# Optimization experiments

Hardware: AMD Instinct MI355X
Metric: run time of the kernel (lower is better)

Reference implementation:

```python
import jax, jax.numpy as jnp
import numpy as np
from jax import lax


def setup_inputs() -> dict:
    key = jax.random.key(0)
    k1, k2 = jax.random.split(key)
    B, H, W, Cin, Cout, kh, kw = 16, 128, 128, 128, 128, 3, 3
    X = jax.random.normal(k1, (B, H, W, Cin), dtype=jnp.float32)
    kernel = jax.random.normal(k2, (B, kh, kw, Cin, Cout), dtype=jnp.float32) * 0.05
    return {"X": X, "kernel": kernel}


def _conv_one(x, k):
    # x: [H, W, Cin]; k: [kh, kw, Cin, Cout] -> [H', W', Cout]
    out = lax.conv_general_dilated(
        x[None],  # [1, H, W, Cin]
        k,
        window_strides=(1, 1),
        padding='VALID',
        dimension_numbers=('NHWC', 'HWIO', 'NHWC'),
    )
    return out[0]


def reference(X, kernel):
    # Per-sample dynamic-filter conv: each batch element convolved with its own
    # [kh, kw, Cin, Cout] filter. Equivalent to the TF depthwise-reshape trick
    # followed by reduce_sum over the input-channel axis.
    return jax.vmap(_conv_one)(X, kernel)  # [B, H', W', Cout]
```

## Files before the change

### kernel.cpp

```cpp
#include <hip/hip_runtime.h>
#include <cstdint>

#define OWD 126
#define MTOT 15876

typedef short bf16x8 __attribute__((ext_vector_type(8)));
typedef float f32x4  __attribute__((ext_vector_type(4)));

#define BT_ELEMS  (16u * 128u * 1152u)
#define XBF_ELEMS (16u * 128u * 128u * 128u)
#define WS_NEEDED ((size_t)(BT_ELEMS + XBF_ELEMS) * 2)

__device__ __forceinline__ uint16_t f2bf(float f) {
    union { float f; uint32_t u; } v;
    v.f = f;
    uint32_t u = v.u;
    return (uint16_t)((u + 0x7FFFu + ((u >> 16) & 1u)) >> 16);
}

__device__ __forceinline__ uint32_t pk2(float a, float b) {
    return (uint32_t)f2bf(a) | ((uint32_t)f2bf(b) << 16);
}

__device__ __forceinline__ void gl_lds16(const uint16_t* g, uint16_t* l) {
    __builtin_amdgcn_global_load_lds(
        (const __attribute__((address_space(1))) uint32_t*)g,
        (__attribute__((address_space(3))) uint32_t*)l, 16, 0, 0);
}

__global__ __launch_bounds__(256) void kprep(const float* __restrict__ Kin,
                                             uint16_t* __restrict__ Bt) {
    const int rs = blockIdx.x;
    const int b  = blockIdx.y;
    const int t  = threadIdx.x;
    const int n  = t & 127;
    const int og = t >> 7;

    const float* src = Kin + (((size_t)b * 9 + rs) << 14);
    uint16_t*    dst = Bt + ((size_t)b * 128 + n) * 1152 + rs * 128;

#pragma unroll
    for (int o = 0; o < 8; ++o) {
        const int oct = og * 8 + o;
        const float* s0 = src + (oct * 8) * 128 + n;
        uint4 p;
        p.x = pk2(s0[0 * 128], s0[1 * 128]);
        p.y = pk2(s0[2 * 128], s0[3 * 128]);
        p.z = pk2(s0[4 * 128], s0[5 * 128]);
        p.w = pk2(s0[6 * 128], s0[7 * 128]);
        *(uint4*)(dst + oct * 8) = p;
    }
}

__global__ __launch_bounds__(256) void xprep(const float* __restrict__ X,
                                             uint16_t* __restrict__ Xbf) {
    const size_t i = ((size_t)blockIdx.x * 256 + threadIdx.x) * 8;
    const float4 a = *(const float4*)(X + i);
    const float4 b = *(const float4*)(X + i + 4);
    uint4 p;
    p.x = pk2(a.x, a.y);
    p.y = pk2(a.z, a.w);
    p.z = pk2(b.x, b.y);
    p.w = pk2(b.z, b.w);
    *(uint4*)(Xbf + i) = p;
}

__global__ __launch_bounds__(256) void conv_mfma_a(const uint16_t* __restrict__ Xbf,
                                                   const uint16_t* __restrict__ Bt,
                                                   float* __restrict__ Out) {
    __shared__ __align__(16) uint16_t lA[2][128 * 64];
    __shared__ __align__(16) uint16_t lB[2][128 * 64];

    const int mtile = blockIdx.x;
    const int b     = blockIdx.y;
    const int tid   = threadIdx.x;
    const int lane  = tid & 63;
    const int wave  = tid >> 6;
    const int wm    = (wave & 1) << 6;
    const int wn    = (wave >> 1) << 6;
    const int l15   = lane & 15;
    const int quad  = lane >> 4;

    const int kc = (lane & 7) ^ (lane >> 3);
    const uint16_t* Asrc[4];
    const uint16_t* Bsrc[4];
#pragma unroll
    for (int i = 0; i < 4; ++i) {
        const int row = wave * 32 + i * 8 + (lane >> 3);
        int m = mtile * 128 + row;
        if (m >= MTOT) m = MTOT - 1;
        const int oh = m / OWD, ow = m - oh * OWD;
        Asrc[i] = Xbf + (((size_t)b * 128 + oh) * 128 + ow) * 128 + kc * 8;
        Bsrc[i] = Bt + ((size_t)b * 128 + row) * 1152 + kc * 8;
    }
    const int dbase = (wave * 256 + lane) * 8;

    f32x4 acc[4][4];
#pragma unroll
    for (int i = 0; i < 4; ++i)
#pragma unroll
        for (int j = 0; j < 4; ++j)
            acc[i][j] = (f32x4){0.f, 0.f, 0.f, 0.f};

#define STAGE(t_, bu_)                                                      \
    {                                                                       \
        const int rs_ = (t_) >> 1;                                         \
        const int c0_ = ((t_) & 1) << 6;                                   \
        const int r_  = (rs_ * 11) >> 5;                \
        const int s_  = rs_ - r_ * 3;                                      \
        const int ao_ = (r_ * 128 + s_) * 128 + c0_;                       \
        const int bo_ = rs_ * 128 + c0_;                                   \
        uint16_t* Ad_ = &lA[bu_][dbase];                                   \
        uint16_t* Bd_ = &lB[bu_][dbase];                                   \
        _Pragma("unroll")                                                  \
        for (int i_ = 0; i_ < 4; ++i_) {                                   \
            gl_lds16(Asrc[i_] + ao_, Ad_ + i_ * 512);                      \
            gl_lds16(Bsrc[i_] + bo_, Bd_ + i_ * 512);                      \
        }                                                                  \
    }

#define COMPUTE(bu_)                                                        \
    {                                                                       \
        _Pragma("unroll")                                                  \
        for (int ksub_ = 0; ksub_ < 2; ++ksub_) {                          \
            bf16x8 af[4], bfr[4];                                          \
            _Pragma("unroll")                                              \
            for (int i_ = 0; i_ < 4; ++i_) {                               \
                const int row_ = wm + i_ * 16 + l15;                       \
                const int pc_  = (ksub_ * 4 + quad) ^ (row_ & 7);          \
                af[i_] = *(const bf16x8*)&lA[bu_][row_ * 64 + pc_ * 8];    \
            }                                                              \
            _Pragma("unroll")                                              \
            for (int j_ = 0; j_ < 4; ++j_) {                               \
                const int row_ = wn + j_ * 16 + l15;                       \
                const int pc_  = (ksub_ * 4 + quad) ^ (row_ & 7);          \
                bfr[j_] = *(const bf16x8*)&lB[bu_][row_ * 64 + pc_ * 8];   \
            }                                                              \
            _Pragma("unroll")                                              \
            for (int i_ = 0; i_ < 4; ++i_)                                 \
                _Pragma("unroll")                                          \
                for (int j_ = 0; j_ < 4; ++j_)                             \
                    acc[i_][j_] = __builtin_amdgcn_mfma_f32_16x16x32_bf16( \
                        af[i_], bfr[j_], acc[i_][j_], 0, 0, 0);            \
        }                                                                  \
    }

    STAGE(0, 0);
    __syncthreads();

#pragma unroll 1
    for (int t = 0; t < 16; t += 2) {
        STAGE(t + 1, 1);
        COMPUTE(0);
        __syncthreads();
        STAGE(t + 2, 0);
        COMPUTE(1);
        __syncthreads();
    }
    STAGE(17, 1);
    COMPUTE(0);
    __syncthreads();
    COMPUTE(1);

#undef STAGE
#undef COMPUTE

#pragma unroll
    for (int i = 0; i < 4; ++i) {
#pragma unroll
        for (int rr = 0; rr < 4; ++rr) {
            const int mrow = mtile * 128 + wm + i * 16 + quad * 4 + rr;
            if (mrow < MTOT) {
                const int oh2 = mrow / OWD;
                const int ow2 = mrow - oh2 * OWD;
                float* op = Out + (((size_t)b * OWD + oh2) * OWD + ow2) * 128 + wn + l15;
#pragma unroll
                for (int j = 0; j < 4; ++j)
                    op[j * 16] = acc[i][j][rr];
            }
        }
    }
}

__global__ __launch_bounds__(256) void conv_mfma(const float* __restrict__ X,
                                                 const uint16_t* __restrict__ Bt,
                                                 float* __restrict__ Out) {
    __shared__ __align__(16) uint16_t lA[128 * 64];
    __shared__ __align__(16) uint16_t lB[128 * 64];

    const int mtile = blockIdx.x;
    const int b     = blockIdx.y;
    const int tid   = threadIdx.x;
    const int lane  = tid & 63;
    const int wave  = tid >> 6;
    const int wm    = (wave & 1) << 6;
    const int wn    = (wave >> 1) << 6;
    const int l15   = lane & 15;
    const int quad  = lane >> 4;

    const int srow  = tid >> 1;
    const int shalf = tid & 1;

    int m = mtile * 128 + srow;
    if (m >= MTOT) m = MTOT - 1;
    const int oh = m / OWD;
    const int ow = m - oh * OWD;
    const float*    Xb = X + (((size_t)b * 128 + oh) * 128 + ow) * 128;
    const uint16_t* Bb = Bt + ((size_t)b * 128 + srow) * 1152 + shalf * 32;

    f32x4 acc[4][4];
#pragma unroll
    for (int i = 0; i < 4; ++i)
#pragma unroll
        for (int j = 0; j < 4; ++j)
            acc[i][j] = (f32x4){0.f, 0.f, 0.f, 0.f};

    for (int chunk = 0; chunk < 18; ++chunk) {
        const int rs = chunk >> 1;
        const int c0 = (chunk & 1) << 6;
        const int r  = rs / 3;
        const int s  = rs - r * 3;

        __syncthreads();
        {
            const float4* src = (const float4*)(Xb + (r * 128 + s) * 128 + c0 + shalf * 32);
            float4 v[8];
#pragma unroll
            for (int i = 0; i < 8; ++i) v[i] = src[i];
#pragma unroll
            for (int i = 0; i < 4; ++i) {
                uint4 p;
                p.x = pk2(v[2 * i].x, v[2 * i].y);
                p.y = pk2(v[2 * i].z, v[2 * i].w);
                p.z = pk2(v[2 * i + 1].x, v[2 * i + 1].y);
                p.w = pk2(v[2 * i + 1].z, v[2 * i + 1].w);
                const int ci = (shalf * 4 + i) ^ (srow & 7);
                *(uint4*)&lA[srow * 64 + ci * 8] = p;
            }
        }
        {
            const uint4* bsrc = (const uint4*)(Bb + rs * 128 + c0);
#pragma unroll
            for (int i = 0; i < 4; ++i) {
                const uint4 p = bsrc[i];
                const int ci = (shalf * 4 + i) ^ (srow & 7);
                *(uint4*)&lB[srow * 64 + ci * 8] = p;
            }
        }
        __syncthreads();

#pragma unroll
        for (int ksub = 0; ksub < 2; ++ksub) {
            bf16x8 af[4], bfr[4];
#pragma unroll
            for (int i = 0; i < 4; ++i) {
                const int row = wm + i * 16 + l15;
                const int ci  = (ksub * 4 + quad) ^ (row & 7);
                af[i] = *(const bf16x8*)&lA[row * 64 + ci * 8];
            }
#pragma unroll
            for (int j = 0; j < 4; ++j) {
                const int row = wn + j * 16 + l15;
                const int ci  = (ksub * 4 + quad) ^ (row & 7);
                bfr[j] = *(const bf16x8*)&lB[row * 64 + ci * 8];
            }
#pragma unroll
            for (int i = 0; i < 4; ++i)
#pragma unroll
                for (int j = 0; j < 4; ++j)
                    acc[i][j] = __builtin_amdgcn_mfma_f32_16x16x32_bf16(
                        af[i], bfr[j], acc[i][j], 0, 0, 0);
        }
    }

#pragma unroll
    for (int i = 0; i < 4; ++i) {
#pragma unroll
        for (int rr = 0; rr < 4; ++rr) {
            const int mrow = mtile * 128 + wm + i * 16 + quad * 4 + rr;
            if (mrow < MTOT) {
                const int oh2 = mrow / OWD;
                const int ow2 = mrow - oh2 * OWD;
                float* op = Out + (((size_t)b * OWD + oh2) * OWD + ow2) * 128 + wn + l15;
#pragma unroll
                for (int j = 0; j < 4; ++j)
                    op[j * 16] = acc[i][j][rr];
            }
        }
    }
}

extern "C" void kernel_launch(void* const* d_in, const int* in_sizes, int n_in,
                              void* d_out, int out_size, void* d_ws, size_t ws_size,
                              hipStream_t stream) {
    const float* X   = (const float*)d_in[0];
    const float* Kin = (const float*)d_in[1];
    float*       Out = (float*)d_out;
    uint16_t*    Bt  = (uint16_t*)d_ws;
    uint16_t*    Xbf = Bt + BT_ELEMS;

    kprep<<<dim3(9, 16), 256, 0, stream>>>(Kin, Bt);
    if (ws_size >= WS_NEEDED) {
        xprep<<<XBF_ELEMS / (256 * 8), 256, 0, stream>>>(X, Xbf);
        conv_mfma_a<<<dim3(125, 16), 256, 0, stream>>>(Xbf, Bt, Out);
    } else {
        conv_mfma<<<dim3(125, 16), 256, 0, stream>>>(X, Bt, Out);
    }
}
```

Baseline: 324.6 us.

## Enlarge M tile to 256 and load B fragments directly into registers

Result: slower. 347.6 us (+7.1%).

```diff
diff --git a/kernel.cpp b/kernel.cpp
--- a/kernel.cpp
+++ b/kernel.cpp
@@ -65,11 +65,142 @@
     *(uint4*)(Xbf + i) = p;
 }
 
-__global__ __launch_bounds__(256) void conv_mfma_a(const uint16_t* __restrict__ Xbf,
-                                                   const uint16_t* __restrict__ Bt,
-                                                   float* __restrict__ Out) {
-    __shared__ __align__(16) uint16_t lA[2][128 * 64];
-    __shared__ __align__(16) uint16_t lB[2][128 * 64];
+__global__ __launch_bounds__(256, 2) void conv_mfma_b(const uint16_t* __restrict__ Xbf,
+                                                      const uint16_t* __restrict__ Bt,
+                                                      float* __restrict__ Out) {
+    __shared__ __align__(16) uint16_t lA[2][256 * 64];
+
+    const int mtile = blockIdx.x;
+    const int b     = blockIdx.y;
+    const int tid   = threadIdx.x;
+    const int lane  = tid & 63;
+    const int wave  = tid >> 6;
+    const int wm    = (wave & 1) << 7;
+    const int wn    = (wave >> 1) << 6;
+    const int l15   = lane & 15;
+    const int quad  = lane >> 4;
+
+    const int kc = (lane & 7) ^ (lane >> 3);
+    const uint16_t* Asrc[8];
+#pragma unroll
+    for (int i = 0; i < 8; ++i) {
+        const int row = wave * 64 + i * 8 + (lane >> 3);
+        int m = mtile * 256 + row;
+        if (m >= MTOT) m = MTOT - 1;
+        const int oh = m / OWD, ow = m - oh * OWD;
+        Asrc[i] = Xbf + (((size_t)b * 128 + oh) * 128 + ow) * 128 + kc * 8;
+    }
+    uint16_t* Ad0 = &lA[0][(wave * 512 + lane) * 8];
+    uint16_t* Ad1 = &lA[1][(wave * 512 + lane) * 8];
+
+    const uint16_t* Bp[4];
+#pragma unroll
+    for (int j = 0; j < 4; ++j)
+        Bp[j] = Bt + ((size_t)b * 128 + wn + j * 16 + l15) * 1152 + quad * 8;
+
+    f32x4 acc[8][4];
+#pragma unroll
+    for (int i = 0; i < 8; ++i)
+#pragma unroll
+        for (int j = 0; j < 4; ++j)
+            acc[i][j] = (f32x4){0.f, 0.f, 0.f, 0.f};
+
+    bf16x8 bA[8], bB[8];
+
+#define STAGE(t_, Ad_)                                                      \
+    {                                                                       \
+        const int rs_ = (t_) >> 1;                                         \
+        const int c0_ = ((t_) & 1) << 6;                                   \
+        const int r_  = (rs_ * 11) >> 5;                \
+        const int s_  = rs_ - r_ * 3;                                      \
+        const int ao_ = (r_ * 128 + s_) * 128 + c0_;                       \
+        _Pragma("unroll")                                                  \
+        for (int i_ = 0; i_ < 8; ++i_)                                     \
+            gl_lds16(Asrc[i_] + ao_, Ad_ + i_ * 512);                      \
+    }
+
+#define LOADB(t_, br_)                                                      \
+    {                                                                       \
+        const int off_ = ((t_) >> 1) * 128 + (((t_) & 1) << 6);            \
+        _Pragma("unroll")                                                  \
+        for (int j_ = 0; j_ < 4; ++j_) {                                   \
+            br_[j_ * 2 + 0] = *(const bf16x8*)(Bp[j_] + off_);             \
+            br_[j_ * 2 + 1] = *(const bf16x8*)(Bp[j_] + off_ + 32);        \
+        }                                                                  \
+    }
+
+#define COMPUTE(bu_, br_)                                                   \
+    {                                                                       \
+        _Pragma("unroll")                                                  \
+        for (int ksub_ = 0; ksub_ < 2; ++ksub_) {                          \
+            _Pragma("unroll")                                              \
+            for (int ih_ = 0; ih_ < 2; ++ih_) {                            \
+                bf16x8 af[4];                                              \
+                _Pragma("unroll")                                          \
+                for (int i_ = 0; i_ < 4; ++i_) {                           \
+                    const int row_ = wm + (ih_ * 4 + i_) * 16 + l15;       \
+                    const int pc_  = (ksub_ * 4 + quad) ^ (row_ & 7);      \
+                    af[i_] = *(const bf16x8*)&lA[bu_][row_ * 64 + pc_ * 8];\
+                }                                                          \
+                _Pragma("unroll")                                          \
+                for (int i_ = 0; i_ < 4; ++i_)                             \
+                    _Pragma("unroll")                                      \
+                    for (int j_ = 0; j_ < 4; ++j_)                         \
+                        acc[ih_ * 4 + i_][j_] =                            \
+                            __builtin_amdgcn_mfma_f32_16x16x32_bf16(       \
+                                af[i_], br_[j_ * 2 + ksub_],               \
+                                acc[ih_ * 4 + i_][j_], 0, 0, 0);           \
+            }                                                              \
+        }                                                                  \
+    }
+
+    LOADB(0, bA);
+    STAGE(0, Ad0);
+    __syncthreads();
+
+#pragma unroll 1
+    for (int t = 0; t < 16; t += 2) {
+        LOADB(t + 1, bB);
+        STAGE(t + 1, Ad1);
+        COMPUTE(0, bA);
+        __syncthreads();
+        LOADB(t + 2, bA);
+        STAGE(t + 2, Ad0);
+        COMPUTE(1, bB);
+        __syncthreads();
+    }
+    LOADB(17, bB);
+    STAGE(17, Ad1);
+    COMPUTE(0, bA);
+    __syncthreads();
+    COMPUTE(1, bB);
+
+#undef STAGE
+#undef LOADB
+#undef COMPUTE
+
+#pragma unroll
+    for (int i = 0; i < 8; ++i) {
+#pragma unroll
+        for (int rr = 0; rr < 4; ++rr) {
+            const int mrow = mtile * 256 + wm + i * 16 + quad * 4 + rr;
+            if (mrow < MTOT) {
+                const int oh2 = mrow / OWD;
+                const int ow2 = mrow - oh2 * OWD;
+                float* op = Out + (((size_t)b * OWD + oh2) * OWD + ow2) * 128 + wn + l15;
+#pragma unroll
+                for (int j = 0; j < 4; ++j)
+                    op[j * 16] = acc[i][j][rr];
+            }
+        }
+    }
+}
+
+__global__ __launch_bounds__(256) void conv_mfma(const float* __restrict__ X,
+                                                 const uint16_t* __restrict__ Bt,
+                                                 float* __restrict__ Out) {
+    __shared__ __align__(16) uint16_t lA[128 * 64];
+    __shared__ __align__(16) uint16_t lB[128 * 64];
 
     const int mtile = blockIdx.x;
     const int b     = blockIdx.y;
@@ -81,123 +212,6 @@
     const int l15   = lane & 15;
     const int quad  = lane >> 4;
 
-    const int kc = (lane & 7) ^ (lane >> 3);
-    const uint16_t* Asrc[4];
-    const uint16_t* Bsrc[4];
-#pragma unroll
-    for (int i = 0; i < 4; ++i) {
-        const int row = wave * 32 + i * 8 + (lane >> 3);
-        int m = mtile * 128 + row;
-        if (m >= MTOT) m = MTOT - 1;
-        const int oh = m / OWD, ow = m - oh * OWD;
-        Asrc[i] = Xbf + (((size_t)b * 128 + oh) * 128 + ow) * 128 + kc * 8;
-        Bsrc[i] = Bt + ((size_t)b * 128 + row) * 1152 + kc * 8;
-    }
-    const int dbase = (wave * 256 + lane) * 8;
-
-    f32x4 acc[4][4];
-#pragma unroll
-    for (int i = 0; i < 4; ++i)
-#pragma unroll
-        for (int j = 0; j < 4; ++j)
-            acc[i][j] = (f32x4){0.f, 0.f, 0.f, 0.f};
-
-#define STAGE(t_, bu_)                                                      \
-    {                                                                       \
-        const int rs_ = (t_) >> 1;                                         \
-        const int c0_ = ((t_) & 1) << 6;                                   \
-        const int r_  = (rs_ * 11) >> 5;                \
-        const int s_  = rs_ - r_ * 3;                                      \
-        const int ao_ = (r_ * 128 + s_) * 128 + c0_;                       \
-        const int bo_ = rs_ * 128 + c0_;                                   \
-        uint16_t* Ad_ = &lA[bu_][dbase];                                   \
-        uint16_t* Bd_ = &lB[bu_][dbase];                                   \
-        _Pragma("unroll")                                                  \
-        for (int i_ = 0; i_ < 4; ++i_) {                                   \
-            gl_lds16(Asrc[i_] + ao_, Ad_ + i_ * 512);                      \
-            gl_lds16(Bsrc[i_] + bo_, Bd_ + i_ * 512);                      \
-        }                                                                  \
-    }
-
-#define COMPUTE(bu_)                                                        \
-    {                                                                       \
-        _Pragma("unroll")                                                  \
-        for (int ksub_ = 0; ksub_ < 2; ++ksub_) {                          \
-            bf16x8 af[4], bfr[4];                                          \
-            _Pragma("unroll")                                              \
-            for (int i_ = 0; i_ < 4; ++i_) {                               \
-                const int row_ = wm + i_ * 16 + l15;                       \
-                const int pc_  = (ksub_ * 4 + quad) ^ (row_ & 7);          \
-                af[i_] = *(const bf16x8*)&lA[bu_][row_ * 64 + pc_ * 8];    \
-            }                                                              \
-            _Pragma("unroll")                                              \
-            for (int j_ = 0; j_ < 4; ++j_) {                               \
-                const int row_ = wn + j_ * 16 + l15;                       \
-                const int pc_  = (ksub_ * 4 + quad) ^ (row_ & 7);          \
-                bfr[j_] = *(const bf16x8*)&lB[bu_][row_ * 64 + pc_ * 8];   \
-            }                                                              \
-            _Pragma("unroll")                                              \
-            for (int i_ = 0; i_ < 4; ++i_)                                 \
-                _Pragma("unroll")                                          \
-                for (int j_ = 0; j_ < 4; ++j_)                             \
-                    acc[i_][j_] = __builtin_amdgcn_mfma_f32_16x16x32_bf16( \
-                        af[i_], bfr[j_], acc[i_][j_], 0, 0, 0);            \
-        }                                                                  \
-    }
-
-    STAGE(0, 0);
-    __syncthreads();
-
-#pragma unroll 1
-    for (int t = 0; t < 16; t += 2) {
-        STAGE(t + 1, 1);
-        COMPUTE(0);
-        __syncthreads();
-        STAGE(t + 2, 0);
-        COMPUTE(1);
-        __syncthreads();
-    }
-    STAGE(17, 1);
-    COMPUTE(0);
-    __syncthreads();
-    COMPUTE(1);
-
-#undef STAGE
-#undef COMPUTE
-
-#pragma unroll
-    for (int i = 0; i < 4; ++i) {
-#pragma unroll
-        for (int rr = 0; rr < 4; ++rr) {
-            const int mrow = mtile * 128 + wm + i * 16 + quad * 4 + rr;
-            if (mrow < MTOT) {
-                const int oh2 = mrow / OWD;
-                const int ow2 = mrow - oh2 * OWD;
-                float* op = Out + (((size_t)b * OWD + oh2) * OWD + ow2) * 128 + wn + l15;
-#pragma unroll
-                for (int j = 0; j < 4; ++j)
-                    op[j * 16] = acc[i][j][rr];
-            }
-        }
-    }
-}
-
-__global__ __launch_bounds__(256) void conv_mfma(const float* __restrict__ X,
-                                                 const uint16_t* __restrict__ Bt,
-                                                 float* __restrict__ Out) {
-    __shared__ __align__(16) uint16_t lA[128 * 64];
-    __shared__ __align__(16) uint16_t lB[128 * 64];
-
-    const int mtile = blockIdx.x;
-    const int b     = blockIdx.y;
-    const int tid   = threadIdx.x;
-    const int lane  = tid & 63;
-    const int wave  = tid >> 6;
-    const int wm    = (wave & 1) << 6;
-    const int wn    = (wave >> 1) << 6;
-    const int l15   = lane & 15;
-    const int quad  = lane >> 4;
-
     const int srow  = tid >> 1;
     const int shalf = tid & 1;
 
@@ -302,7 +316,7 @@
     kprep<<<dim3(9, 16), 256, 0, stream>>>(Kin, Bt);
     if (ws_size >= WS_NEEDED) {
         xprep<<<XBF_ELEMS / (256 * 8), 256, 0, stream>>>(X, Xbf);
-        conv_mfma_a<<<dim3(125, 16), 256, 0, stream>>>(Xbf, Bt, Out);
+        conv_mfma_b<<<dim3(63, 16), 256, 0, stream>>>(Xbf, Bt, Out);
     } else {
         conv_mfma<<<dim3(125, 16), 256, 0, stream>>>(X, Bt, Out);
     }
```

## Use triple-buffered K=32 LDS pipeline with vmcnt waits and XCD-aware block remap

Applied to the files above, without the earlier changes.

Result: no change. 325.8 us (+0.4%).

```diff
diff --git a/kernel.cpp b/kernel.cpp
--- a/kernel.cpp
+++ b/kernel.cpp
@@ -65,11 +65,142 @@
     *(uint4*)(Xbf + i) = p;
 }
 
-__global__ __launch_bounds__(256) void conv_mfma_a(const uint16_t* __restrict__ Xbf,
+__global__ __launch_bounds__(256) void conv_mfma_c(const uint16_t* __restrict__ Xbf,
                                                    const uint16_t* __restrict__ Bt,
                                                    float* __restrict__ Out) {
-    __shared__ __align__(16) uint16_t lA[2][128 * 64];
-    __shared__ __align__(16) uint16_t lB[2][128 * 64];
+    __shared__ __align__(16) uint16_t lds[3][256 * 32];
+
+    const int id    = blockIdx.x + 125 * blockIdx.y;
+    const int nid   = (id & 7) * 250 + (id >> 3);
+    const int mtile = nid % 125;
+    const int b     = nid / 125;
+
+    const int tid  = threadIdx.x;
+    const int lane = tid & 63;
+    const int wave = tid >> 6;
+    const int wm   = (wave & 1) << 6;
+    const int wn   = (wave >> 1) << 6;
+    const int l15  = lane & 15;
+    const int quad = lane >> 4;
+
+    const int l2 = lane >> 2;
+    const int kc = (lane & 3) ^ (l2 & 3);
+    const uint16_t* Asrc[2];
+    const uint16_t* Bsrc[2];
+#pragma unroll
+    for (int i = 0; i < 2; ++i) {
+        const int row = wave * 32 + i * 16 + l2;
+        int m = mtile * 128 + row;
+        if (m >= MTOT) m = MTOT - 1;
+        const int oh = m / OWD, ow = m - oh * OWD;
+        Asrc[i] = Xbf + (((size_t)b * 128 + oh) * 128 + ow) * 128 + kc * 8;
+        Bsrc[i] = Bt + ((size_t)b * 128 + row) * 1152 + kc * 8;
+    }
+    const int dbase = wave * 1024 + lane * 8;
+
+    f32x4 acc[4][4];
+#pragma unroll
+    for (int i = 0; i < 4; ++i)
+#pragma unroll
+        for (int j = 0; j < 4; ++j)
+            acc[i][j] = (f32x4){0.f, 0.f, 0.f, 0.f};
+
+#define STAGE(t_, bu_)                                                      \
+    {                                                                       \
+        const int rs_ = (t_) >> 2;                                         \
+        const int c0_ = ((t_) & 3) << 5;                                   \
+        const int r_  = (rs_ * 11) >> 5;                \
+        const int s_  = rs_ - r_ * 3;                                      \
+        const int ao_ = (r_ * 128 + s_) * 128 + c0_;                       \
+        const int bo_ = rs_ * 128 + c0_;                                   \
+        uint16_t* Ad_ = &lds[bu_][dbase];                                  \
+        uint16_t* Bd_ = &lds[bu_][4096 + dbase];                           \
+        _Pragma("unroll")                                                  \
+        for (int i_ = 0; i_ < 2; ++i_) {                                   \
+            gl_lds16(Asrc[i_] + ao_, Ad_ + i_ * 512);                      \
+            gl_lds16(Bsrc[i_] + bo_, Bd_ + i_ * 512);                      \
+        }                                                                  \
+    }
+
+#define COMPUTE(bu_)                                                        \
+    {                                                                       \
+        bf16x8 af[4], bfr[4];                                              \
+        _Pragma("unroll")                                                  \
+        for (int i_ = 0; i_ < 4; ++i_) {                                   \
+            const int row_ = wm + i_ * 16 + l15;                           \
+            const int sl_  = quad ^ (row_ & 3);                            \
+            af[i_] = *(const bf16x8*)&lds[bu_][row_ * 32 + sl_ * 8];       \
+        }                                                                  \
+        _Pragma("unroll")                                                  \
+        for (int j_ = 0; j_ < 4; ++j_) {                                   \
+            const int row_ = wn + j_ * 16 + l15;                           \
+            const int sl_  = quad ^ (row_ & 3);                            \
+            bfr[j_] = *(const bf16x8*)&lds[bu_][4096 + row_ * 32 + sl_ * 8];\
+        }                                                                  \
+        _Pragma("unroll")                                                  \
+        for (int i_ = 0; i_ < 4; ++i_)                                     \
+            _Pragma("unroll")                                              \
+            for (int j_ = 0; j_ < 4; ++j_)                                 \
+                acc[i_][j_] = __builtin_amdgcn_mfma_f32_16x16x32_bf16(     \
+                    af[i_], bfr[j_], acc[i_][j_], 0, 0, 0);                \
+    }
+
+#define WAITBAR4                                                            \
+    asm volatile("s_waitcnt vmcnt(4)" ::: "memory");                       \
+    __builtin_amdgcn_s_barrier();                                          \
+    __builtin_amdgcn_sched_barrier(0);
+
+#define ITER(t_, bc_, bs_)                                                  \
+    {                                                                       \
+        WAITBAR4;                                                          \
+        STAGE((t_) + 2, bs_);                                              \
+        COMPUTE(bc_);                                                      \
+    }
+
+    STAGE(0, 0);
+    STAGE(1, 1);
+
+#pragma unroll 1
+    for (int t = 0; t < 33; t += 3) {
+        ITER(t, 0, 2);
+        ITER(t + 1, 1, 0);
+        ITER(t + 2, 2, 1);
+    }
+    ITER(33, 0, 2);
+    WAITBAR4;
+    COMPUTE(1);
+    asm volatile("s_waitcnt vmcnt(0)" ::: "memory");
+    __builtin_amdgcn_s_barrier();
+    __builtin_amdgcn_sched_barrier(0);
+    COMPUTE(2);
+
+#undef STAGE
+#undef COMPUTE
+#undef WAITBAR4
+#undef ITER
+
+#pragma unroll
+    for (int i = 0; i < 4; ++i) {
+#pragma unroll
+        for (int rr = 0; rr < 4; ++rr) {
+            const int mrow = mtile * 128 + wm + i * 16 + quad * 4 + rr;
+            if (mrow < MTOT) {
+                const int oh2 = mrow / OWD;
+                const int ow2 = mrow - oh2 * OWD;
+                float* op = Out + (((size_t)b * OWD + oh2) * OWD + ow2) * 128 + wn + l15;
+#pragma unroll
+                for (int j = 0; j < 4; ++j)
+                    op[j * 16] = acc[i][j][rr];
+            }
+        }
+    }
+}
+
+__global__ __launch_bounds__(256) void conv_mfma(const float* __restrict__ X,
+                                                 const uint16_t* __restrict__ Bt,
+                                                 float* __restrict__ Out) {
+    __shared__ __align__(16) uint16_t lA[128 * 64];
+    __shared__ __align__(16) uint16_t lB[128 * 64];
 
     const int mtile = blockIdx.x;
     const int b     = blockIdx.y;
@@ -81,123 +212,6 @@
     const int l15   = lane & 15;
     const int quad  = lane >> 4;
 
-    const int kc = (lane & 7) ^ (lane >> 3);
-    const uint16_t* Asrc[4];
-    const uint16_t* Bsrc[4];
-#pragma unroll
-    for (int i = 0; i < 4; ++i) {
-        const int row = wave * 32 + i * 8 + (lane >> 3);
-        int m = mtile * 128 + row;
-        if (m >= MTOT) m = MTOT - 1;
-        const int oh = m / OWD, ow = m - oh * OWD;
-        Asrc[i] = Xbf + (((size_t)b * 128 + oh) * 128 + ow) * 128 + kc * 8;
-        Bsrc[i] = Bt + ((size_t)b * 128 + row) * 1152 + kc * 8;
-    }
-    const int dbase = (wave * 256 + lane) * 8;
-
-    f32x4 acc[4][4];
-#pragma unroll
-    for (int i = 0; i < 4; ++i)
-#pragma unroll
-        for (int j = 0; j < 4; ++j)
-            acc[i][j] = (f32x4){0.f, 0.f, 0.f, 0.f};
-
-#define STAGE(t_, bu_)                                                      \
-    {                                                                       \
-        const int rs_ = (t_) >> 1;                                         \
-        const int c0_ = ((t_) & 1) << 6;                                   \
-        const int r_  = (rs_ * 11) >> 5;                \
-        const int s_  = rs_ - r_ * 3;                                      \
-        const int ao_ = (r_ * 128 + s_) * 128 + c0_;                       \
-        const int bo_ = rs_ * 128 + c0_;                                   \
-        uint16_t* Ad_ = &lA[bu_][dbase];                                   \
-        uint16_t* Bd_ = &lB[bu_][dbase];                                   \
-        _Pragma("unroll")                                                  \
-        for (int i_ = 0; i_ < 4; ++i_) {                                   \
-            gl_lds16(Asrc[i_] + ao_, Ad_ + i_ * 512);                      \
-            gl_lds16(Bsrc[i_] + bo_, Bd_ + i_ * 512);                      \
-        }                                                                  \
-    }
-
-#define COMPUTE(bu_)                                                        \
-    {                                                                       \
-        _Pragma("unroll")                                                  \
-        for (int ksub_ = 0; ksub_ < 2; ++ksub_) {                          \
-            bf16x8 af[4], bfr[4];                                          \
-            _Pragma("unroll")                                              \
-            for (int i_ = 0; i_ < 4; ++i_) {                               \
-                const int row_ = wm + i_ * 16 + l15;                       \
-                const int pc_  = (ksub_ * 4 + quad) ^ (row_ & 7);          \
-                af[i_] = *(const bf16x8*)&lA[bu_][row_ * 64 + pc_ * 8];    \
-            }                                                              \
-            _Pragma("unroll")                                              \
-            for (int j_ = 0; j_ < 4; ++j_) {                               \
-                const int row_ = wn + j_ * 16 + l15;                       \
-                const int pc_  = (ksub_ * 4 + quad) ^ (row_ & 7);          \
-                bfr[j_] = *(const bf16x8*)&lB[bu_][row_ * 64 + pc_ * 8];   \
-            }                                                              \
-            _Pragma("unroll")                                              \
-            for (int i_ = 0; i_ < 4; ++i_)                                 \
-                _Pragma("unroll")                                          \
-                for (int j_ = 0; j_ < 4; ++j_)                             \
-                    acc[i_][j_] = __builtin_amdgcn_mfma_f32_16x16x32_bf16( \
-                        af[i_], bfr[j_], acc[i_][j_], 0, 0, 0);            \
-        }                                                                  \
-    }
-
-    STAGE(0, 0);
-    __syncthreads();
-
-#pragma unroll 1
-    for (int t = 0; t < 16; t += 2) {
-        STAGE(t + 1, 1);
-        COMPUTE(0);
-        __syncthreads();
-        STAGE(t + 2, 0);
-        COMPUTE(1);
-        __syncthreads();
-    }
-    STAGE(17, 1);
-    COMPUTE(0);
-    __syncthreads();
-    COMPUTE(1);
-
-#undef STAGE
-#undef COMPUTE
-
-#pragma unroll
-    for (int i = 0; i < 4; ++i) {
-#pragma unroll
-        for (int rr = 0; rr < 4; ++rr) {
-            const int mrow = mtile * 128 + wm + i * 16 + quad * 4 + rr;
-            if (mrow < MTOT) {
-                const int oh2 = mrow / OWD;
-                const int ow2 = mrow - oh2 * OWD;
-                float* op = Out + (((size_t)b * OWD + oh2) * OWD + ow2) * 128 + wn + l15;
-#pragma unroll
-                for (int j = 0; j < 4; ++j)
-                    op[j * 16] = acc[i][j][rr];
-            }
-        }
-    }
-}
-
-__global__ __launch_bounds__(256) void conv_mfma(const float* __restrict__ X,
-                                                 const uint16_t* __restrict__ Bt,
-                                                 float* __restrict__ Out) {
-    __shared__ __align__(16) uint16_t lA[128 * 64];
-    __shared__ __align__(16) uint16_t lB[128 * 64];
-
-    const int mtile = blockIdx.x;
-    const int b     = blockIdx.y;
-    const int tid   = threadIdx.x;
-    const int lane  = tid & 63;
-    const int wave  = tid >> 6;
-    const int wm    = (wave & 1) << 6;
-    const int wn    = (wave >> 1) << 6;
-    const int l15   = lane & 15;
-    const int quad  = lane >> 4;
-
     const int srow  = tid >> 1;
     const int shalf = tid & 1;
 
@@ -302,7 +316,7 @@
     kprep<<<dim3(9, 16), 256, 0, stream>>>(Kin, Bt);
     if (ws_size >= WS_NEEDED) {
         xprep<<<XBF_ELEMS / (256 * 8), 256, 0, stream>>>(X, Xbf);
-        conv_mfma_a<<<dim3(125, 16), 256, 0, stream>>>(Xbf, Bt, Out);
+        conv_mfma_c<<<dim3(125, 16), 256, 0, stream>>>(Xbf, Bt, Out);
     } else {
         conv_mfma<<<dim3(125, 16), 256, 0, stream>>>(X, Bt, Out);
     }
```
